# Kernel optimization log

Measured on AMD Instinct MI355X. Metric: run time of the kernel, lower is better.

## Reference

```python
import jax, jax.numpy as jnp
import numpy as np


def setup_inputs() -> dict:
    key = jax.random.key(0)
    x = jax.random.normal(key, (8, 256, 16384), dtype=jnp.float32)
    gamma = jnp.zeros((1,), dtype=jnp.float32)
    return {"x": x, "gamma": gamma}


def reference(x, gamma):
    # x: (B, C, T)
    # energy[b, i, j] = sum_t x[b, i, t] * x[b, j, t]  -> (B, C, C)
    energy = jnp.einsum('bit,bjt->bij', x, x)
    # max-subtract trick: attention = softmax(max_j(energy) - energy)
    energy_new = jnp.max(energy, axis=-1, keepdims=True) - energy
    attention = jax.nn.softmax(energy_new, axis=-1)
    # out[b, i, t] = sum_j attention[b, i, j] * x[b, j, t]
    out = jnp.einsum('bij,bjt->bit', attention, x)
    return gamma * out + x
```

## Files before the change

kernel.cpp:

```cpp
#include <hip/hip_runtime.h>
#include <hip/hip_bf16.h>

#define NB 8
#define NC 256
#define NT 16384

using bf16x8 = __attribute__((ext_vector_type(8))) __bf16;
using f32x16 = __attribute__((ext_vector_type(16))) float;
using f32x4  = __attribute__((ext_vector_type(4))) float;
using u32x4  = __attribute__((ext_vector_type(4))) unsigned int;

__device__ __forceinline__ unsigned short bf16_rne(float f) {
  unsigned int u = __float_as_uint(f);
  u += 0x7FFFu + ((u >> 16) & 1u);
  return (unsigned short)(u >> 16);
}

__device__ __forceinline__ unsigned int pack_bf16_pair_rne(float f_lo, float f_hi) {
  unsigned int a = __float_as_uint(f_lo), b = __float_as_uint(f_hi);
  a += 0x7FFFu + ((a >> 16) & 1u);
  b += 0x7FFFu + ((b >> 16) & 1u);
  return __builtin_amdgcn_perm(b, a, 0x07060302u);
}

template <int ITERS>
__global__ __launch_bounds__(1024) void k_gram(const float* __restrict__ x,
                                               float* __restrict__ Gp) {
  __shared__ __align__(16) unsigned short lds[256 * 72];
  const int b   = blockIdx.y;
  const int kc  = blockIdx.x;
  const int tid = threadIdx.x;
  const int l   = tid & 63, w = tid >> 6;
  const int wr  = w >> 2, wc = w & 3;
  const int l31 = l & 31, lh = l >> 5;

  const float* __restrict__ xb = x + (size_t)b * NC * NT;

  const int sr = tid >> 2;
  const int sq = tid & 3;
  const float* sp = xb + (size_t)sr * NT + kc * (ITERS * 64) + sq * 16;

  f32x4 r0 = ((const f32x4*)sp)[0];
  f32x4 r1 = ((const f32x4*)sp)[1];
  f32x4 r2 = ((const f32x4*)sp)[2];
  f32x4 r3 = ((const f32x4*)sp)[3];

  f32x16 acc00, acc01, acc10, acc11;
#pragma unroll
  for (int i = 0; i < 16; ++i) { acc00[i] = 0.f; acc01[i] = 0.f; acc10[i] = 0.f; acc11[i] = 0.f; }

#pragma unroll 1
  for (int it = 0; it < ITERS; ++it) {
    __syncthreads();
    u32x4 p0, p1;
    p0[0] = pack_bf16_pair_rne(r0[0], r0[1]); p0[1] = pack_bf16_pair_rne(r0[2], r0[3]);
    p0[2] = pack_bf16_pair_rne(r1[0], r1[1]); p0[3] = pack_bf16_pair_rne(r1[2], r1[3]);
    p1[0] = pack_bf16_pair_rne(r2[0], r2[1]); p1[1] = pack_bf16_pair_rne(r2[2], r2[3]);
    p1[2] = pack_bf16_pair_rne(r3[0], r3[1]); p1[3] = pack_bf16_pair_rne(r3[2], r3[3]);
    u32x4* dst = (u32x4*)&lds[sr * 72 + sq * 16];
    dst[0] = p0;
    dst[1] = p1;
    if (it < ITERS - 1) {
      const float* np = sp + (it + 1) * 64;
      r0 = ((const f32x4*)np)[0]; r1 = ((const f32x4*)np)[1];
      r2 = ((const f32x4*)np)[2]; r3 = ((const f32x4*)np)[3];
    }
    __syncthreads();
#pragma unroll
    for (int s = 0; s < 4; ++s) {
      const int ko = s * 16 + lh * 8;
      bf16x8 a0 = *(const bf16x8*)&lds[(wr * 64 +      l31) * 72 + ko];
      bf16x8 a1 = *(const bf16x8*)&lds[(wr * 64 + 32 + l31) * 72 + ko];
      bf16x8 b0 = *(const bf16x8*)&lds[(wc * 64 +      l31) * 72 + ko];
      bf16x8 b1 = *(const bf16x8*)&lds[(wc * 64 + 32 + l31) * 72 + ko];
      acc00 = __builtin_amdgcn_mfma_f32_32x32x16_bf16(a0, b0, acc00, 0, 0, 0);
      acc01 = __builtin_amdgcn_mfma_f32_32x32x16_bf16(a0, b1, acc01, 0, 0, 0);
      acc10 = __builtin_amdgcn_mfma_f32_32x32x16_bf16(a1, b0, acc10, 0, 0, 0);
      acc11 = __builtin_amdgcn_mfma_f32_32x32x16_bf16(a1, b1, acc11, 0, 0, 0);
    }
  }

  float* __restrict__ Gb = Gp + ((size_t)kc * NB + b) * NC * NC;
  const int ibase = wr * 64 + 4 * lh;
  const int jbase = wc * 64 + l31;
#pragma unroll
  for (int g = 0; g < 16; ++g) {
    const int ir = (g & 3) + 8 * (g >> 2);
    Gb[(ibase + ir) * NC      + jbase     ] = acc00[g];
    Gb[(ibase + ir) * NC      + jbase + 32] = acc01[g];
    Gb[(ibase + 32 + ir) * NC + jbase     ] = acc10[g];
    Gb[(ibase + 32 + ir) * NC + jbase + 32] = acc11[g];
  }
}

template <int NKC>
__global__ __launch_bounds__(256) void k_softmax(const float* __restrict__ Gp,
                                                 const float* __restrict__ gamma,
                                                 unsigned short* __restrict__ Att) {
  const int row = blockIdx.x * 4 + (threadIdx.x >> 6);
  const int l   = threadIdx.x & 63;
  const int i   = row & (NC - 1);
  const float* base = Gp + (size_t)row * NC + l * 4;

  f32x4 v; v[0] = 0.f; v[1] = 0.f; v[2] = 0.f; v[3] = 0.f;
#pragma unroll
  for (int kc = 0; kc < NKC; ++kc) {
    f32x4 p = *(const f32x4*)(base + (size_t)kc * (NB * NC * NC));
    v[0] += p[0]; v[1] += p[1]; v[2] += p[2]; v[3] += p[3];
  }

  float mn = fminf(fminf(v[0], v[1]), fminf(v[2], v[3]));
#pragma unroll
  for (int m = 32; m >= 1; m >>= 1) mn = fminf(mn, __shfl_xor(mn, m, 64));
  float p0 = __expf(mn - v[0]), p1 = __expf(mn - v[1]);
  float p2 = __expf(mn - v[2]), p3 = __expf(mn - v[3]);
  float s = (p0 + p1) + (p2 + p3);
#pragma unroll
  for (int m = 32; m >= 1; m >>= 1) s += __shfl_xor(s, m, 64);
  const float sc = gamma[0] / s;

  const int j0 = 4 * l;
  ushort4 o;
  o.x = bf16_rne(p0 * sc + ((j0 + 0) == i ? 1.f : 0.f));
  o.y = bf16_rne(p1 * sc + ((j0 + 1) == i ? 1.f : 0.f));
  o.z = bf16_rne(p2 * sc + ((j0 + 2) == i ? 1.f : 0.f));
  o.w = bf16_rne(p3 * sc + ((j0 + 3) == i ? 1.f : 0.f));
  *(ushort4*)(Att + (size_t)row * NC + j0) = o;
}

__global__ __launch_bounds__(1024) void k_out(const float* __restrict__ x,
                                              const unsigned short* __restrict__ Att,
                                              float* __restrict__ y) {
  __shared__ __align__(16) float bs[32 * 260];
  __shared__ __align__(16) unsigned short as_[256 * 40];
  const int b   = blockIdx.y;
  const int t0  = blockIdx.x * 256;
  const int tid = threadIdx.x;
  const int l   = tid & 63, w = tid >> 6;
  const int rbw = w >> 3, cbw = w & 7;
  const int l31 = l & 31, lh = l >> 5;

  const float* __restrict__ xb = x + (size_t)b * NC * NT;
  const unsigned short* __restrict__ Ab = Att + (size_t)b * NC * NC;

  const int bk = tid >> 5, bf = tid & 31;
  const int ar = tid >> 2, aseg = tid & 3;

  const float* bsp = xb + (size_t)bk * NT + t0 + bf * 4;
  f32x4 rb0 = *(const f32x4*)bsp;
  f32x4 rb1 = *(const f32x4*)(bsp + 128);
  u32x4 ra  = *(const u32x4*)(Ab + ar * NC + aseg * 8);

  f32x16 acc0, acc1, acc2, acc3;
#pragma unroll
  for (int i = 0; i < 16; ++i) { acc0[i] = 0.f; acc1[i] = 0.f; acc2[i] = 0.f; acc3[i] = 0.f; }

#pragma unroll 1
  for (int it = 0; it < 8; ++it) {
    __syncthreads();
    *(f32x4*)&bs[bk * 260 + bf * 4]       = rb0;
    *(f32x4*)&bs[bk * 260 + 128 + bf * 4] = rb1;
    *(u32x4*)&as_[ar * 40 + aseg * 8]     = ra;
    if (it < 7) {
      const float* np = bsp + (size_t)(it + 1) * 32 * NT;
      rb0 = *(const f32x4*)np;
      rb1 = *(const f32x4*)(np + 128);
      ra  = *(const u32x4*)(Ab + ar * NC + (it + 1) * 32 + aseg * 8);
    }
    __syncthreads();
#pragma unroll
    for (int s = 0; s < 2; ++s) {
      const int kr = s * 16 + lh * 8;
      const int tc = cbw * 32 + l31;
      float f0 = bs[(kr + 0) * 260 + tc], f1 = bs[(kr + 1) * 260 + tc];
      float f2 = bs[(kr + 2) * 260 + tc], f3 = bs[(kr + 3) * 260 + tc];
      float f4 = bs[(kr + 4) * 260 + tc], f5 = bs[(kr + 5) * 260 + tc];
      float f6 = bs[(kr + 6) * 260 + tc], f7 = bs[(kr + 7) * 260 + tc];
      u32x4 pk;
      pk[0] = pack_bf16_pair_rne(f0, f1); pk[1] = pack_bf16_pair_rne(f2, f3);
      pk[2] = pack_bf16_pair_rne(f4, f5); pk[3] = pack_bf16_pair_rne(f6, f7);
      bf16x8 bfrag = __builtin_bit_cast(bf16x8, pk);
      const int ao = s * 16 + lh * 8;
      bf16x8 a0 = *(const bf16x8*)&as_[(rbw * 128 +      l31) * 40 + ao];
      bf16x8 a1 = *(const bf16x8*)&as_[(rbw * 128 + 32 + l31) * 40 + ao];
      bf16x8 a2 = *(const bf16x8*)&as_[(rbw * 128 + 64 + l31) * 40 + ao];
      bf16x8 a3 = *(const bf16x8*)&as_[(rbw * 128 + 96 + l31) * 40 + ao];
      acc0 = __builtin_amdgcn_mfma_f32_32x32x16_bf16(a0, bfrag, acc0, 0, 0, 0);
      acc1 = __builtin_amdgcn_mfma_f32_32x32x16_bf16(a1, bfrag, acc1, 0, 0, 0);
      acc2 = __builtin_amdgcn_mfma_f32_32x32x16_bf16(a2, bfrag, acc2, 0, 0, 0);
      acc3 = __builtin_amdgcn_mfma_f32_32x32x16_bf16(a3, bfrag, acc3, 0, 0, 0);
    }
  }

  const int tg = t0 + cbw * 32 + l31;
  const int ib = rbw * 128 + 4 * lh;
#pragma unroll
  for (int g = 0; g < 16; ++g) {
    const int ir = (g & 3) + 8 * (g >> 2);
    size_t i0 = (size_t)(b * NC + ib + ir) * NT + tg;
    y[i0] = acc0[g];
    y[i0 + (size_t)32 * NT] = acc1[g];
    y[i0 + (size_t)64 * NT] = acc2[g];
    y[i0 + (size_t)96 * NT] = acc3[g];
  }
}

extern "C" void kernel_launch(void* const* d_in, const int* in_sizes, int n_in,
                              void* d_out, int out_size, void* d_ws, size_t ws_size,
                              hipStream_t stream) {
  const float* x     = (const float*)d_in[0];
  const float* gamma = (const float*)d_in[1];
  float* y = (float*)d_out;

  const size_t chunk_bytes = (size_t)NB * NC * NC * sizeof(float);
  const size_t att_bytes   = (size_t)NB * NC * NC * sizeof(unsigned short);

  int nkc;
  if      (ws_size >= 32 * chunk_bytes + att_bytes) nkc = 32;
  else if (ws_size >= 16 * chunk_bytes + att_bytes) nkc = 16;
  else if (ws_size >=  8 * chunk_bytes + att_bytes) nkc = 8;
  else                                              nkc = 4;

  float* Gp = (float*)d_ws;
  unsigned short* Att = (unsigned short*)((char*)d_ws + (size_t)nkc * chunk_bytes);

  switch (nkc) {
    case 32:
      k_gram<8>  <<<dim3(32, NB), 1024, 0, stream>>>(x, Gp);
      k_softmax<32><<<dim3(NB * NC / 4), 256, 0, stream>>>(Gp, gamma, Att);
      break;
    case 16:
      k_gram<16> <<<dim3(16, NB), 1024, 0, stream>>>(x, Gp);
      k_softmax<16><<<dim3(NB * NC / 4), 256, 0, stream>>>(Gp, gamma, Att);
      break;
    case 8:
      k_gram<32> <<<dim3(8, NB), 1024, 0, stream>>>(x, Gp);
      k_softmax<8><<<dim3(NB * NC / 4), 256, 0, stream>>>(Gp, gamma, Att);
      break;
    default:
      k_gram<64> <<<dim3(4, NB), 1024, 0, stream>>>(x, Gp);
      k_softmax<4><<<dim3(NB * NC / 4), 256, 0, stream>>>(Gp, gamma, Att);
      break;
  }
  k_out<<<dim3(NT / 256, NB), 1024, 0, stream>>>(x, Att, y);
}
```

Measured before the change: 283.0 us.

## Shrink k_out tile to 64 columns with 256 threads and vectorize Gram stores

k_out now processes 64 time columns per block with 256 threads. Each wave computes a 64x64 output tile, two row-blocks by two column-blocks, which gives four times as many blocks and lighter LDS use per block, aiming at better occupancy and latency hiding. Each thread now loads a whole 32-element attention row segment. The Gram epilogue writes the transposed partial tile with 16-byte vector stores instead of scalar stores, relying on the Gram matrix being symmetric. The smaller tile reuses each converted bf16 x fragment across only two MFMAs instead of four, which may add LDS traffic and conversion work.

```diff
diff --git a/kernel.cpp b/kernel.cpp
--- a/kernel.cpp
+++ b/kernel.cpp
@@ -81,15 +81,20 @@
   }
 
   float* __restrict__ Gb = Gp + ((size_t)kc * NB + b) * NC * NC;
-  const int ibase = wr * 64 + 4 * lh;
-  const int jbase = wc * 64 + l31;
-#pragma unroll
-  for (int g = 0; g < 16; ++g) {
-    const int ir = (g & 3) + 8 * (g >> 2);
-    Gb[(ibase + ir) * NC      + jbase     ] = acc00[g];
-    Gb[(ibase + ir) * NC      + jbase + 32] = acc01[g];
-    Gb[(ibase + 32 + ir) * NC + jbase     ] = acc10[g];
-    Gb[(ibase + 32 + ir) * NC + jbase + 32] = acc11[g];
+  float* r0p = &Gb[(wc * 64 + l31) * NC + wr * 64 + 4 * lh];
+  float* r1p = r0p + 32 * NC;
+#pragma unroll
+  for (int q = 0; q < 4; ++q) {
+    f32x4 v00, v01, v10, v11;
+#pragma unroll
+    for (int r = 0; r < 4; ++r) {
+      v00[r] = acc00[4 * q + r]; v01[r] = acc01[4 * q + r];
+      v10[r] = acc10[4 * q + r]; v11[r] = acc11[4 * q + r];
+    }
+    *(f32x4*)(r0p + 8 * q)      = v00;
+    *(f32x4*)(r0p + 32 + 8 * q) = v10;
+    *(f32x4*)(r1p + 8 * q)      = v01;
+    *(f32x4*)(r1p + 32 + 8 * q) = v11;
   }
 }
 
@@ -128,28 +133,30 @@
   *(ushort4*)(Att + (size_t)row * NC + j0) = o;
 }
 
-__global__ __launch_bounds__(1024) void k_out(const float* __restrict__ x,
-                                              const unsigned short* __restrict__ Att,
-                                              float* __restrict__ y) {
-  __shared__ __align__(16) float bs[32 * 260];
+__global__ __launch_bounds__(256) void k_out(const float* __restrict__ x,
+                                             const unsigned short* __restrict__ Att,
+                                             float* __restrict__ y) {
+  __shared__ __align__(16) float bs[32 * 68];
   __shared__ __align__(16) unsigned short as_[256 * 40];
   const int b   = blockIdx.y;
-  const int t0  = blockIdx.x * 256;
+  const int t0  = blockIdx.x * 64;
   const int tid = threadIdx.x;
   const int l   = tid & 63, w = tid >> 6;
-  const int rbw = w >> 3, cbw = w & 7;
   const int l31 = l & 31, lh = l >> 5;
 
   const float* __restrict__ xb = x + (size_t)b * NC * NT;
   const unsigned short* __restrict__ Ab = Att + (size_t)b * NC * NC;
 
-  const int bk = tid >> 5, bf = tid & 31;
-  const int ar = tid >> 2, aseg = tid & 3;
-
-  const float* bsp = xb + (size_t)bk * NT + t0 + bf * 4;
+  const int bk = tid >> 3, bq = tid & 7;
+  const float* bsp = xb + (size_t)bk * NT + t0 + bq * 4;
+  const unsigned short* asp = Ab + (size_t)tid * NC;
+
   f32x4 rb0 = *(const f32x4*)bsp;
-  f32x4 rb1 = *(const f32x4*)(bsp + 128);
-  u32x4 ra  = *(const u32x4*)(Ab + ar * NC + aseg * 8);
+  f32x4 rb1 = *(const f32x4*)(bsp + 32);
+  u32x4 ra0 = *(const u32x4*)(asp + 0);
+  u32x4 ra1 = *(const u32x4*)(asp + 8);
+  u32x4 ra2 = *(const u32x4*)(asp + 16);
+  u32x4 ra3 = *(const u32x4*)(asp + 24);
 
   f32x16 acc0, acc1, acc2, acc3;
 #pragma unroll
@@ -158,50 +165,59 @@
 #pragma unroll 1
   for (int it = 0; it < 8; ++it) {
     __syncthreads();
-    *(f32x4*)&bs[bk * 260 + bf * 4]       = rb0;
-    *(f32x4*)&bs[bk * 260 + 128 + bf * 4] = rb1;
-    *(u32x4*)&as_[ar * 40 + aseg * 8]     = ra;
+    *(f32x4*)&bs[bk * 68 + bq * 4]      = rb0;
+    *(f32x4*)&bs[bk * 68 + 32 + bq * 4] = rb1;
+    *(u32x4*)&as_[tid * 40 + 0]  = ra0;
+    *(u32x4*)&as_[tid * 40 + 8]  = ra1;
+    *(u32x4*)&as_[tid * 40 + 16] = ra2;
+    *(u32x4*)&as_[tid * 40 + 24] = ra3;
     if (it < 7) {
       const float* np = bsp + (size_t)(it + 1) * 32 * NT;
       rb0 = *(const f32x4*)np;
-      rb1 = *(const f32x4*)(np + 128);
-      ra  = *(const u32x4*)(Ab + ar * NC + (it + 1) * 32 + aseg * 8);
+      rb1 = *(const f32x4*)(np + 32);
+      const unsigned short* na = asp + (it + 1) * 32;
+      ra0 = *(const u32x4*)(na + 0);
+      ra1 = *(const u32x4*)(na + 8);
+      ra2 = *(const u32x4*)(na + 16);
+      ra3 = *(const u32x4*)(na + 24);
     }
     __syncthreads();
 #pragma unroll
     for (int s = 0; s < 2; ++s) {
       const int kr = s * 16 + lh * 8;
-      const int tc = cbw * 32 + l31;
-      float f0 = bs[(kr + 0) * 260 + tc], f1 = bs[(kr + 1) * 260 + tc];
-      float f2 = bs[(kr + 2) * 260 + tc], f3 = bs[(kr + 3) * 260 + tc];
-      float f4 = bs[(kr + 4) * 260 + tc], f5 = bs[(kr + 5) * 260 + tc];
-      float f6 = bs[(kr + 6) * 260 + tc], f7 = bs[(kr + 7) * 260 + tc];
-      u32x4 pk;
-      pk[0] = pack_bf16_pair_rne(f0, f1); pk[1] = pack_bf16_pair_rne(f2, f3);
-      pk[2] = pack_bf16_pair_rne(f4, f5); pk[3] = pack_bf16_pair_rne(f6, f7);
-      bf16x8 bfrag = __builtin_bit_cast(bf16x8, pk);
       const int ao = s * 16 + lh * 8;
-      bf16x8 a0 = *(const bf16x8*)&as_[(rbw * 128 +      l31) * 40 + ao];
-      bf16x8 a1 = *(const bf16x8*)&as_[(rbw * 128 + 32 + l31) * 40 + ao];
-      bf16x8 a2 = *(const bf16x8*)&as_[(rbw * 128 + 64 + l31) * 40 + ao];
-      bf16x8 a3 = *(const bf16x8*)&as_[(rbw * 128 + 96 + l31) * 40 + ao];
-      acc0 = __builtin_amdgcn_mfma_f32_32x32x16_bf16(a0, bfrag, acc0, 0, 0, 0);
-      acc1 = __builtin_amdgcn_mfma_f32_32x32x16_bf16(a1, bfrag, acc1, 0, 0, 0);
-      acc2 = __builtin_amdgcn_mfma_f32_32x32x16_bf16(a2, bfrag, acc2, 0, 0, 0);
-      acc3 = __builtin_amdgcn_mfma_f32_32x32x16_bf16(a3, bfrag, acc3, 0, 0, 0);
-    }
-  }
-
-  const int tg = t0 + cbw * 32 + l31;
-  const int ib = rbw * 128 + 4 * lh;
+      bf16x8 a0 = *(const bf16x8*)&as_[(w * 64 +      l31) * 40 + ao];
+      bf16x8 a1 = *(const bf16x8*)&as_[(w * 64 + 32 + l31) * 40 + ao];
+#pragma unroll
+      for (int tb = 0; tb < 2; ++tb) {
+        const int tc = tb * 32 + l31;
+        float f0 = bs[(kr + 0) * 68 + tc], f1 = bs[(kr + 1) * 68 + tc];
+        float f2 = bs[(kr + 2) * 68 + tc], f3 = bs[(kr + 3) * 68 + tc];
+        float f4 = bs[(kr + 4) * 68 + tc], f5 = bs[(kr + 5) * 68 + tc];
+        float f6 = bs[(kr + 6) * 68 + tc], f7 = bs[(kr + 7) * 68 + tc];
+        u32x4 pk;
+        pk[0] = pack_bf16_pair_rne(f0, f1); pk[1] = pack_bf16_pair_rne(f2, f3);
+        pk[2] = pack_bf16_pair_rne(f4, f5); pk[3] = pack_bf16_pair_rne(f6, f7);
+        bf16x8 bfrag = __builtin_bit_cast(bf16x8, pk);
+        if (tb == 0) {
+          acc0 = __builtin_amdgcn_mfma_f32_32x32x16_bf16(a0, bfrag, acc0, 0, 0, 0);
+          acc2 = __builtin_amdgcn_mfma_f32_32x32x16_bf16(a1, bfrag, acc2, 0, 0, 0);
+        } else {
+          acc1 = __builtin_amdgcn_mfma_f32_32x32x16_bf16(a0, bfrag, acc1, 0, 0, 0);
+          acc3 = __builtin_amdgcn_mfma_f32_32x32x16_bf16(a1, bfrag, acc3, 0, 0, 0);
+        }
+      }
+    }
+  }
+
 #pragma unroll
   for (int g = 0; g < 16; ++g) {
-    const int ir = (g & 3) + 8 * (g >> 2);
-    size_t i0 = (size_t)(b * NC + ib + ir) * NT + tg;
-    y[i0] = acc0[g];
-    y[i0 + (size_t)32 * NT] = acc1[g];
-    y[i0 + (size_t)64 * NT] = acc2[g];
-    y[i0 + (size_t)96 * NT] = acc3[g];
+    const int ir = (g & 3) + 8 * (g >> 2) + 4 * lh;
+    size_t i0 = (size_t)(b * NC + w * 64 + ir) * NT + t0 + l31;
+    y[i0]                            = acc0[g];
+    y[i0 + 32]                       = acc1[g];
+    y[i0 + (size_t)32 * NT]          = acc2[g];
+    y[i0 + (size_t)32 * NT + 32]     = acc3[g];
   }
 }
 
@@ -242,5 +258,5 @@
       k_softmax<4><<<dim3(NB * NC / 4), 256, 0, stream>>>(Gp, gamma, Att);
       break;
   }
-  k_out<<<dim3(NT / 256, NB), 1024, 0, stream>>>(x, Att, y);
-}
+  k_out<<<dim3(NT / 64, NB), 256, 0, stream>>>(x, Att, y);
+}
```

Measured after the change: 309.9 us. +9.5%, slower.
